# Optimization experiments

Measured on AMD Instinct MI355X. Metric: run time of the kernel, lower is better.

The kernel has to match this reference:

```python
import jax, jax.numpy as jnp
import numpy as np
import math

HIDDEN = 8
HEADS = 2
HEAD_DIM = HIDDEN // HEADS  # 4
MAX_SEQ = 102
B, S = 4096, 102


def _rotary_cache(seq_len, head_dim):
    # Matches _create_rotary_embeddings: dim = head_dim//2, inv_freq over arange(0, dim, 2)
    pos = jnp.arange(seq_len, dtype=jnp.float32)
    dim = head_dim // 2
    inv_freq = 1.0 / (10000.0 ** (jnp.arange(0, dim, 2, dtype=jnp.float32) / dim))
    sinusoid = pos[:, None] * inv_freq[None, :]           # [seq, dim//2] -> [102, 1]
    return jnp.stack([jnp.sin(sinusoid), jnp.cos(sinusoid)], axis=0)  # [2, seq, 1]


def _apply_rotary(x, cos, sin):
    # x: [B, H, S, hd]; cos/sin: [2, S, 1] (faithful to the source's buggy unpack,
    # which broadcasts the stacked sin/cos pair across the H==2 head dim)
    x2 = jnp.stack([-x[..., 1::2], x[..., ::2]], axis=-1).reshape(x.shape)
    return x * cos + x2 * sin


def setup_inputs() -> dict:
    key = jax.random.key(0)
    kq, kk, kv, k1, k2, k3, k4 = jax.random.split(key, 7)
    scale = 1.0 / math.sqrt(HIDDEN)
    return {
        "query": jax.random.normal(kq, (B, S, HIDDEN), dtype=jnp.float32),
        "key": jax.random.normal(kk, (B, S, HIDDEN), dtype=jnp.float32),
        "value": jax.random.normal(kv, (B, S, HIDDEN), dtype=jnp.float32),
        "wq": jax.random.normal(k1, (HIDDEN, HIDDEN), dtype=jnp.float32) * scale,
        "wk": jax.random.normal(k2, (HIDDEN, HIDDEN), dtype=jnp.float32) * scale,
        "wv": jax.random.normal(k3, (HIDDEN, HIDDEN), dtype=jnp.float32) * scale,
        "wo": jax.random.normal(k4, (HIDDEN, HIDDEN), dtype=jnp.float32) * scale,
    }


def reference(query, key, value, wq, wk, wv, wo):
    b, sq, _ = query.shape
    sk = key.shape[1]
    # nn.Linear (no bias): y = x @ W^T
    q = query @ wq.T
    k = key @ wk.T
    v = value @ wv.T
    # b n (h d) -> b h n d
    def split_heads(t, s):
        return t.reshape(b, s, HEADS, HEAD_DIM).transpose(0, 2, 1, 3)
    q = split_heads(q, sq)
    k = split_heads(k, sk)
    v = split_heads(v, sk)
    cache = _rotary_cache(MAX_SEQ, HEAD_DIM)
    sin_t = cache[:, :sq]  # [2, sq, 1] (named 'sin' in source, holds stacked sin/cos)
    cos_t = cache[:, :sk]  # [2, sk, 1]
    q = _apply_rotary(q, cos_t, sin_t)
    k = _apply_rotary(k, cos_t, sin_t)
    scale = 1.0 / math.sqrt(HEAD_DIM)
    # chunk_size = min(sk, 1024) = sk -> single chunk == full softmax attention
    scores = jnp.einsum('bhqd,bhkd->bhqk', q, k) * scale  # [B, H, Sq, Sk]
    attn = jax.nn.softmax(scores, axis=-1)
    out = jnp.einsum('bhqk,bhkd->bhqd', attn, v)
    # b h n d -> b n (h d)
    out = out.transpose(0, 2, 1, 3).reshape(b, sq, HIDDEN)
    return out @ wo.T
```

## Files before the change

### kernel.cpp

```cpp
#include <hip/hip_runtime.h>

#define NB 4096
#define SS 102
#define HID 8
#define NH 2
#define HD 4

__global__ __launch_bounds__(256, 4) void mha_fused_kernel(
    const float* __restrict__ query, const float* __restrict__ key,
    const float* __restrict__ value, const float* __restrict__ wq,
    const float* __restrict__ wk, const float* __restrict__ wv,
    const float* __restrict__ wo, float* __restrict__ out)
{
    __shared__ float sRaw[3 * SS * HID];
    __shared__ float sP[3 * NH * SS * HD];
    __shared__ float sW[4 * 64];

    const int t = threadIdx.x;
    const int b = blockIdx.x;

    if (t < 64)        sW[t]       = wq[t];
    else if (t < 128)  sW[t]       = wk[t - 64];
    else if (t < 192)  sW[t]       = wv[t - 128];
    else               sW[t]       = wo[t - 192];

    {
        const float4* q4 = (const float4*)(query + (size_t)b * (SS * HID));
        const float4* k4 = (const float4*)(key   + (size_t)b * (SS * HID));
        const float4* v4 = (const float4*)(value + (size_t)b * (SS * HID));
        float4* sRaw4 = (float4*)sRaw;
        if (t < 204) {
            sRaw4[t]           = q4[t];
            sRaw4[204 + t]     = k4[t];
            sRaw4[408 + t]     = v4[t];
        }
    }
    __syncthreads();

    for (int p = t; p < 816; p += 256) {
        const int tensor = p / 408;
        const int pp = p % 408;
        const int s  = pp >> 2;
        const int pr = pp & 3;
        const int i0 = pr * 2, i1 = i0 + 1;
        const float* raw = sRaw + tensor * (SS * HID) + s * HID;
        const float* w   = sW + tensor * 64;
        float x0 = 0.f, x1 = 0.f;
#pragma unroll
        for (int j = 0; j < 8; ++j) {
            x0 += raw[j] * w[i0 * 8 + j];
            x1 += raw[j] * w[i1 * 8 + j];
        }
        const int h = i0 >> 2;
        const float wr = (h == 0) ? sinf((float)s) : cosf((float)s);
        const float r0 = (x0 - x1) * wr;
        const float r1 = (x1 + x0) * wr;
        const int d0 = i0 & 3;
        float* dst = sP + tensor * (NH * SS * HD) + h * (SS * HD) + s * HD + d0;
        dst[0] = r0;
        dst[1] = r1;
    }
    for (int e = t; e < 816; e += 256) {
        const int s = e >> 3, i = e & 7;
        const float* raw = sRaw + 2 * (SS * HID) + s * HID;
        const float* w   = sW + 2 * 64 + i * 8;
        float x = 0.f;
#pragma unroll
        for (int j = 0; j < 8; ++j) x += raw[j] * w[j];
        const int h = i >> 2, d = i & 3;
        sP[2 * (NH * SS * HD) + h * (SS * HD) + s * HD + d] = x;
    }
    __syncthreads();

    float acc0 = 0.f, acc1 = 0.f, acc2 = 0.f, acc3 = 0.f, l = 0.f;
    int h = 0, qr = 0;
    if (t < 204) {
        h = t / SS;
        qr = t - h * SS;
        const float4 qv = *(const float4*)(sP + h * (SS * HD) + qr * HD);
        const float q0 = qv.x * 0.5f, q1 = qv.y * 0.5f,
                    q2 = qv.z * 0.5f, q3 = qv.w * 0.5f;
        const float4* K4 = (const float4*)(sP + 1 * (NH * SS * HD) + h * (SS * HD));
        const float4* V4 = (const float4*)(sP + 2 * (NH * SS * HD) + h * (SS * HD));
        for (int k = 0; k < SS; ++k) {
            const float4 kv = K4[k];
            const float sc = q0 * kv.x + q1 * kv.y + q2 * kv.z + q3 * kv.w;
            const float pterm = __expf(sc);
            const float4 vv = V4[k];
            l += pterm;
            acc0 += pterm * vv.x;
            acc1 += pterm * vv.y;
            acc2 += pterm * vv.z;
            acc3 += pterm * vv.w;
        }
    }
    __syncthreads();
    if (t < 204) {
        const float inv = 1.f / l;
        float* comb = sRaw + qr * HID + h * HD;
        comb[0] = acc0 * inv;
        comb[1] = acc1 * inv;
        comb[2] = acc2 * inv;
        comb[3] = acc3 * inv;
    }
    __syncthreads();

    for (int e = t; e < 816; e += 256) {
        const int s = e >> 3, i = e & 7;
        const float* comb = sRaw + s * HID;
        const float* w    = sW + 3 * 64 + i * 8;
        float x = 0.f;
#pragma unroll
        for (int j = 0; j < 8; ++j) x += comb[j] * w[j];
        out[(size_t)b * (SS * HID) + e] = x;
    }
}

extern "C" void kernel_launch(void* const* d_in, const int* in_sizes, int n_in,
                              void* d_out, int out_size, void* d_ws, size_t ws_size,
                              hipStream_t stream) {
    const float* query = (const float*)d_in[0];
    const float* key   = (const float*)d_in[1];
    const float* value = (const float*)d_in[2];
    const float* wq    = (const float*)d_in[3];
    const float* wk    = (const float*)d_in[4];
    const float* wv    = (const float*)d_in[5];
    const float* wo    = (const float*)d_in[6];
    float* out = (float*)d_out;
    mha_fused_kernel<<<NB, 256, 0, stream>>>(query, key, value, wq, wk, wv, wo, out);
}
```

Measured before the change: 125.4 us.

## Rewrite fused MHA kernel with fp16 packed K/V, split-key attention and exp2

Rewrites the kernel around a new work layout. Each wave computes one full projection per row, with weights read through scalar loads. K and V are stored interleaved as fp16 in LDS. Each lane handles two query rows over half the keys, and the two halves are combined through LDS. The softmax scale is folded with log2(e) into Q so exp2 replaces exp, and the sin/cos table is precomputed once per block. Storing K/V in fp16 reduces precision.

```diff
diff --git a/kernel.cpp b/kernel.cpp
--- a/kernel.cpp
+++ b/kernel.cpp
@@ -2,117 +2,173 @@
 
 #define NB 4096
 #define SS 102
-#define HID 8
-#define NH 2
-#define HD 4
+#define QSCALE 0.72134752044448170368f
 
-__global__ __launch_bounds__(256, 4) void mha_fused_kernel(
+typedef float v2f __attribute__((ext_vector_type(2)));
+typedef __fp16 h2 __attribute__((ext_vector_type(2)));
+typedef __fp16 h8 __attribute__((ext_vector_type(8)));
+
+__global__ __launch_bounds__(256) void mha_fused_kernel(
     const float* __restrict__ query, const float* __restrict__ key,
     const float* __restrict__ value, const float* __restrict__ wq,
-    const float* __restrict__ wk, const float* __restrict__ wv,
+    const float* __restrict__ wk, const float* __restrict__ wvp,
     const float* __restrict__ wo, float* __restrict__ out)
 {
-    __shared__ float sRaw[3 * SS * HID];
-    __shared__ float sP[3 * NH * SS * HD];
-    __shared__ float sW[4 * 64];
+    __shared__ __align__(16) unsigned char lds[17264];
+    float*  RAW  = (float*)lds;
+    float*  QF   = (float*)(lds + 9792);
+    float*  ROTT = (float*)(lds + 13120);
+    __fp16* KV   = (__fp16*)(lds + 13936);
+    float*  COMB = (float*)lds;
+    float*  PART = (float*)(lds + 3264);
 
     const int t = threadIdx.x;
     const int b = blockIdx.x;
 
-    if (t < 64)        sW[t]       = wq[t];
-    else if (t < 128)  sW[t]       = wk[t - 64];
-    else if (t < 192)  sW[t]       = wv[t - 128];
-    else               sW[t]       = wo[t - 192];
+    float4 rq, rk, rv;
+    if (t < 204) {
+        const float4* q4 = (const float4*)(query + (size_t)b * 816);
+        const float4* k4 = (const float4*)(key   + (size_t)b * 816);
+        const float4* v4 = (const float4*)(value + (size_t)b * 816);
+        rq = q4[t]; rk = k4[t]; rv = v4[t];
+    }
+
+    if (t < SS) {
+        const float ang = (float)t;
+        ROTT[2 * t]     = sinf(ang);
+        ROTT[2 * t + 1] = cosf(ang);
+    }
+    if (t >= 208 && t < 212) {
+        const int z = t - 208;
+        *(float4*)(QF + (((z >> 1) * 104) + SS + (z & 1)) * 4) =
+            (float4){0.f, 0.f, 0.f, 0.f};
+    }
+
+    if (t < 204) {
+        float4* R4 = (float4*)RAW;
+        R4[t]       = rq;
+        R4[204 + t] = rk;
+        R4[408 + t] = rv;
+    }
+    __syncthreads();
 
     {
-        const float4* q4 = (const float4*)(query + (size_t)b * (SS * HID));
-        const float4* k4 = (const float4*)(key   + (size_t)b * (SS * HID));
-        const float4* v4 = (const float4*)(value + (size_t)b * (SS * HID));
-        float4* sRaw4 = (float4*)sRaw;
-        if (t < 204) {
-            sRaw4[t]           = q4[t];
-            sRaw4[204 + t]     = k4[t];
-            sRaw4[408 + t]     = v4[t];
+        const int wvu  = __builtin_amdgcn_readfirstlane(t >> 6);
+        const int lane = t & 63;
+        if (wvu < 3) {
+            const float* W = (wvu == 0) ? wq : (wvu == 1) ? wk : wvp;
+            for (int r = lane; r < SS; r += 64) {
+                const float4 a = *(const float4*)(RAW + (wvu * SS + r) * 8);
+                const float4 c = *(const float4*)(RAW + (wvu * SS + r) * 8 + 4);
+                float x[8];
+#pragma unroll
+                for (int ch = 0; ch < 8; ++ch) {
+                    x[ch] = a.x * W[ch * 8 + 0] + a.y * W[ch * 8 + 1]
+                          + a.z * W[ch * 8 + 2] + a.w * W[ch * 8 + 3]
+                          + c.x * W[ch * 8 + 4] + c.y * W[ch * 8 + 5]
+                          + c.z * W[ch * 8 + 6] + c.w * W[ch * 8 + 7];
+                }
+                if (wvu == 2) {
+#pragma unroll
+                    for (int h = 0; h < 2; ++h) {
+                        __fp16* rec = KV + (h * 104 + r) * 8;
+                        *(h2*)(rec + 4) = __builtin_amdgcn_cvt_pkrtz(x[4*h+0], x[4*h+1]);
+                        *(h2*)(rec + 6) = __builtin_amdgcn_cvt_pkrtz(x[4*h+2], x[4*h+3]);
+                    }
+                } else {
+                    const float2 sc = *(const float2*)(ROTT + 2 * r);
+#pragma unroll
+                    for (int h = 0; h < 2; ++h) {
+                        float w = (h == 0) ? sc.x : sc.y;
+                        if (wvu == 0) w *= QSCALE;
+                        const float y0 = (x[4*h+0] - x[4*h+1]) * w;
+                        const float y1 = (x[4*h+1] + x[4*h+0]) * w;
+                        const float y2 = (x[4*h+2] - x[4*h+3]) * w;
+                        const float y3 = (x[4*h+3] + x[4*h+2]) * w;
+                        if (wvu == 0) {
+                            *(float4*)(QF + (h * 104 + r) * 4) =
+                                (float4){y0, y1, y2, y3};
+                        } else {
+                            __fp16* rec = KV + (h * 104 + r) * 8;
+                            *(h2*)(rec)     = __builtin_amdgcn_cvt_pkrtz(y0, y1);
+                            *(h2*)(rec + 2) = __builtin_amdgcn_cvt_pkrtz(y2, y3);
+                        }
+                    }
+                }
+            }
         }
     }
     __syncthreads();
 
-    for (int p = t; p < 816; p += 256) {
-        const int tensor = p / 408;
-        const int pp = p % 408;
-        const int s  = pp >> 2;
-        const int pr = pp & 3;
-        const int i0 = pr * 2, i1 = i0 + 1;
-        const float* raw = sRaw + tensor * (SS * HID) + s * HID;
-        const float* w   = sW + tensor * 64;
-        float x0 = 0.f, x1 = 0.f;
+    {
+        const int wv   = t >> 6, lane = t & 63;
+        const int h    = wv >> 1, kh = wv & 1;
+        const bool act = lane < 52;
+        v2f acc0 = {0.f, 0.f}, acc1 = {0.f, 0.f},
+            acc2 = {0.f, 0.f}, acc3 = {0.f, 0.f}, L = {0.f, 0.f};
+        if (act) {
+            const float4 qa = *(const float4*)(QF + (h * 104 + 2 * lane) * 4);
+            const float4 qc = *(const float4*)(QF + (h * 104 + 2 * lane + 1) * 4);
+            const v2f q0 = {qa.x, qc.x}, q1 = {qa.y, qc.y},
+                      q2 = {qa.z, qc.z}, q3 = {qa.w, qc.w};
+            const __fp16* KVh = KV + (h * 104 + kh * 51) * 8;
+            for (int j = 0; j < 51; ++j) {
+                const h8 rec = *(const h8*)(KVh + j * 8);
+                const float k0 = (float)rec[0], k1 = (float)rec[1];
+                const float k2 = (float)rec[2], k3 = (float)rec[3];
+                const float v0 = (float)rec[4], v1 = (float)rec[5];
+                const float v2 = (float)rec[6], v3 = (float)rec[7];
+                v2f s = q0 * k0 + q1 * k1 + q2 * k2 + q3 * k3;
+                v2f p;
+                p.x = __builtin_amdgcn_exp2f(s.x);
+                p.y = __builtin_amdgcn_exp2f(s.y);
+                L += p;
+                acc0 += p * v0; acc1 += p * v1;
+                acc2 += p * v2; acc3 += p * v3;
+            }
+            if (kh == 1) {
+                float* P = PART + (h * 52 + lane) * 10;
+                *(v2f*)(P + 0) = acc0; *(v2f*)(P + 2) = acc1;
+                *(v2f*)(P + 4) = acc2; *(v2f*)(P + 6) = acc3;
+                *(v2f*)(P + 8) = L;
+            }
+        }
+        __syncthreads();
+        if (act && kh == 0) {
+            const float* P = PART + (h * 52 + lane) * 10;
+            acc0 += *(const v2f*)(P + 0); acc1 += *(const v2f*)(P + 2);
+            acc2 += *(const v2f*)(P + 4); acc3 += *(const v2f*)(P + 6);
+            L    += *(const v2f*)(P + 8);
+            const float a0[2] = {acc0.x, acc0.y}, a1[2] = {acc1.x, acc1.y};
+            const float a2[2] = {acc2.x, acc2.y}, a3[2] = {acc3.x, acc3.y};
+            const float ll[2] = {L.x, L.y};
 #pragma unroll
-        for (int j = 0; j < 8; ++j) {
-            x0 += raw[j] * w[i0 * 8 + j];
-            x1 += raw[j] * w[i1 * 8 + j];
+            for (int j = 0; j < 2; ++j) {
+                const int row = 2 * lane + j;
+                if (row < SS) {
+                    const float inv = 1.f / ll[j];
+                    *(float4*)(COMB + row * 8 + h * 4) =
+                        (float4){a0[j] * inv, a1[j] * inv, a2[j] * inv, a3[j] * inv};
+                }
+            }
         }
-        const int h = i0 >> 2;
-        const float wr = (h == 0) ? sinf((float)s) : cosf((float)s);
-        const float r0 = (x0 - x1) * wr;
-        const float r1 = (x1 + x0) * wr;
-        const int d0 = i0 & 3;
-        float* dst = sP + tensor * (NH * SS * HD) + h * (SS * HD) + s * HD + d0;
-        dst[0] = r0;
-        dst[1] = r1;
-    }
-    for (int e = t; e < 816; e += 256) {
-        const int s = e >> 3, i = e & 7;
-        const float* raw = sRaw + 2 * (SS * HID) + s * HID;
-        const float* w   = sW + 2 * 64 + i * 8;
-        float x = 0.f;
-#pragma unroll
-        for (int j = 0; j < 8; ++j) x += raw[j] * w[j];
-        const int h = i >> 2, d = i & 3;
-        sP[2 * (NH * SS * HD) + h * (SS * HD) + s * HD + d] = x;
     }
     __syncthreads();
 
-    float acc0 = 0.f, acc1 = 0.f, acc2 = 0.f, acc3 = 0.f, l = 0.f;
-    int h = 0, qr = 0;
-    if (t < 204) {
-        h = t / SS;
-        qr = t - h * SS;
-        const float4 qv = *(const float4*)(sP + h * (SS * HD) + qr * HD);
-        const float q0 = qv.x * 0.5f, q1 = qv.y * 0.5f,
-                    q2 = qv.z * 0.5f, q3 = qv.w * 0.5f;
-        const float4* K4 = (const float4*)(sP + 1 * (NH * SS * HD) + h * (SS * HD));
-        const float4* V4 = (const float4*)(sP + 2 * (NH * SS * HD) + h * (SS * HD));
-        for (int k = 0; k < SS; ++k) {
-            const float4 kv = K4[k];
-            const float sc = q0 * kv.x + q1 * kv.y + q2 * kv.z + q3 * kv.w;
-            const float pterm = __expf(sc);
-            const float4 vv = V4[k];
-            l += pterm;
-            acc0 += pterm * vv.x;
-            acc1 += pterm * vv.y;
-            acc2 += pterm * vv.z;
-            acc3 += pterm * vv.w;
+    if (t < SS) {
+        const float4 a = *(const float4*)(COMB + t * 8);
+        const float4 c = *(const float4*)(COMB + t * 8 + 4);
+        float x[8];
+#pragma unroll
+        for (int ch = 0; ch < 8; ++ch) {
+            x[ch] = a.x * wo[ch * 8 + 0] + a.y * wo[ch * 8 + 1]
+                  + a.z * wo[ch * 8 + 2] + a.w * wo[ch * 8 + 3]
+                  + c.x * wo[ch * 8 + 4] + c.y * wo[ch * 8 + 5]
+                  + c.z * wo[ch * 8 + 6] + c.w * wo[ch * 8 + 7];
         }
-    }
-    __syncthreads();
-    if (t < 204) {
-        const float inv = 1.f / l;
-        float* comb = sRaw + qr * HID + h * HD;
-        comb[0] = acc0 * inv;
-        comb[1] = acc1 * inv;
-        comb[2] = acc2 * inv;
-        comb[3] = acc3 * inv;
-    }
-    __syncthreads();
-
-    for (int e = t; e < 816; e += 256) {
-        const int s = e >> 3, i = e & 7;
-        const float* comb = sRaw + s * HID;
-        const float* w    = sW + 3 * 64 + i * 8;
-        float x = 0.f;
-#pragma unroll
-        for (int j = 0; j < 8; ++j) x += comb[j] * w[j];
-        out[(size_t)b * (SS * HID) + e] = x;
+        float* o = out + (size_t)b * 816 + t * 8;
+        *(float4*)(o)     = (float4){x[0], x[1], x[2], x[3]};
+        *(float4*)(o + 4) = (float4){x[4], x[5], x[6], x[7]};
     }
 }
 
```

Result: faster. 122.7 us (-2.2%).
